# Kernel optimization log

Hardware: AMD Instinct MI355X
Metric: run time of the kernel (lower is better)

Reference implementation:

```python
import jax, jax.numpy as jnp
import numpy as np

B, T, C = 8, 2048, 1024
H, S = 16, 64  # heads, head size (R=K=V=S)
HEAD_SIZE_DIVISOR = 8.0
EPS = 1e-5


def setup_inputs() -> dict:
    key = jax.random.key(0)
    ks = jax.random.split(key, 16)
    n = lambda k, shape, s=1.0: jax.random.normal(k, shape, dtype=jnp.float32) * s
    u = lambda k, shape: jax.random.uniform(k, shape, dtype=jnp.float32)
    w_scale = 0.02
    return {
        "xq": n(ks[0], (B, T, C)),
        "xk": n(ks[1], (B, T, C)),
        "xv": n(ks[2], (B, T, C)),
        "time_mix_k": u(ks[3], (1, 1, C)),
        "time_mix_v": u(ks[4], (1, 1, C)),
        "time_mix_r": u(ks[5], (1, 1, C)),
        "time_mix_g": u(ks[6], (1, 1, C)),
        "time_decay": n(ks[7], (H, S)),          # decay speed logits
        "time_faaaa": u(ks[8], (H, S)) * 0.5,     # per-channel bonus
        "Wr": n(ks[9], (C, C), w_scale),
        "Wk": n(ks[10], (C, C), w_scale),
        "Wv": n(ks[11], (C, C), w_scale),
        "Wg": n(ks[12], (C, C), w_scale),
        "Wo": n(ks[13], (C, C), w_scale),
        "ln_w": jnp.ones((C,), jnp.float32),
        "ln_b": jnp.zeros((C,), jnp.float32),
    }


def reference(xq, xk, xv, time_mix_k, time_mix_v, time_mix_r, time_mix_g,
              time_decay, time_faaaa, Wr, Wk, Wv, Wg, Wo, ln_w, ln_b):
    # Note: the torch forward ignores its xk/xv args and rebuilds them from xq.
    x = xq
    Bx, Tx, Cx = x.shape
    # time_shift: shift sequence right by 1, zero-pad first position
    xs = jnp.concatenate([jnp.zeros_like(x[:, :1]), x[:, :-1]], axis=1)
    mix = lambda m: x * m + xs * (1.0 - m)
    # projections (torch Linear: y = x @ W.T), split into heads
    r = (mix(time_mix_r) @ Wr.T).reshape(Bx, Tx, H, S)
    k = (mix(time_mix_k) @ Wk.T).reshape(Bx, Tx, H, S)
    v = (mix(time_mix_v) @ Wv.T).reshape(Bx, Tx, H, S)
    g = jax.nn.silu(mix(time_mix_g) @ Wg.T)  # (B, T, H*S)

    w = jnp.exp(-jnp.exp(time_decay))[None, :, :, None]  # (1,H,K,1) per-k-channel decay in (0,1)
    u = time_faaaa[None, :, :, None]                      # (1,H,K,1) bonus for current token

    def step(s, rkv):
        rt, kt, vt = rkv  # each (B, H, S)
        at = jnp.einsum('bhk,bhv->bhkv', kt, vt)          # outer product
        out = jnp.einsum('bhk,bhkv->bhv', rt, u * at + s)
        return at + w * s, out

    rkv = (jnp.swapaxes(r, 0, 1).swapaxes(1, 2).transpose(0, 1, 2, 3),) if False else None
    r_t = r.transpose(1, 0, 2, 3)  # (T, B, H, S)
    k_t = k.transpose(1, 0, 2, 3)
    v_t = v.transpose(1, 0, 2, 3)
    s0 = jnp.zeros((Bx, H, S, S), dtype=x.dtype)
    _, out = jax.lax.scan(step, s0, (r_t, k_t, v_t))  # out: (T, B, H, S)
    out = out.transpose(1, 0, 2, 3)  # (B, T, H, S)

    # GroupNorm with num_groups=H over channels H*S, applied to out/8
    y = out / HEAD_SIZE_DIVISOR
    mu = y.mean(axis=-1, keepdims=True)
    var = y.var(axis=-1, keepdims=True)
    y = (y - mu) / jnp.sqrt(var + EPS)
    y = y.reshape(Bx, Tx, H * S) * ln_w + ln_b

    return (y * g) @ Wo.T
```

## Files before the change

kernel.cpp:

```cpp
#include <hip/hip_runtime.h>
#include <stdint.h>

using bf16x8 = __attribute__((ext_vector_type(8))) __bf16;
using f32x4  = __attribute__((ext_vector_type(4))) float;

__device__ __forceinline__ unsigned short f2bf(float f) {
  unsigned u = __float_as_uint(f);
  u = u + 0x7FFFu + ((u >> 16) & 1u);
  return (unsigned short)(u >> 16);
}
__device__ __forceinline__ float bf2f(unsigned short h) {
  return __uint_as_float(((unsigned)h) << 16);
}
__device__ __forceinline__ void gload16(const void* g, void* l) {
  __builtin_amdgcn_global_load_lds((const __attribute__((address_space(1))) void*)g,
                                   (__attribute__((address_space(3))) void*)l, 16, 0, 0);
}

__global__ __launch_bounds__(256) void castw_kernel(const float* __restrict__ w,
                                                    unsigned short* __restrict__ o) {
  int i4 = blockIdx.x * 256 + threadIdx.x;
  float4 f = *(const float4*)(w + (size_t)i4 * 4);
  ushort4 u;
  u.x = f2bf(f.x); u.y = f2bf(f.y); u.z = f2bf(f.z); u.w = f2bf(f.w);
  *(ushort4*)(o + (size_t)i4 * 4) = u;
}

__global__ __launch_bounds__(256) void mix1_kernel(const float* __restrict__ x,
                                                   const float* __restrict__ m,
                                                   unsigned short* __restrict__ amix) {
  int idx = blockIdx.x * 256 + threadIdx.x;
  int row = idx >> 8;
  int c0  = (idx & 255) << 2;
  size_t xoff = (size_t)row * 1024 + c0;
  float4 xv = *(const float4*)(x + xoff);
  float4 xs = make_float4(0.f, 0.f, 0.f, 0.f);
  if ((row & 2047) != 0) xs = *(const float4*)(x + xoff - 1024);
  float4 mm = *(const float4*)(m + c0);
  ushort4 u;
  u.x = f2bf(xv.x * mm.x + xs.x * (1.f - mm.x));
  u.y = f2bf(xv.y * mm.y + xs.y * (1.f - mm.y));
  u.z = f2bf(xv.z * mm.z + xs.z * (1.f - mm.z));
  u.w = f2bf(xv.w * mm.w + xs.w * (1.f - mm.w));
  *(ushort4*)(amix + xoff) = u;
}

__global__ __launch_bounds__(256) void gemm_kernel(
    const unsigned short* __restrict__ A,
    const unsigned short* __restrict__ W,
    unsigned short* __restrict__ Cbf,
    float* __restrict__ Cf,
    int do_silu, int f32out) {
  const int brow = blockIdx.y * 128;
  const int bcol = blockIdx.x * 128;
  const int t = threadIdx.x;
  const int lane = t & 63, wv = t >> 6;
  const int wr = wv >> 1, wc = wv & 1;
  const int lm = lane & 15, lk = lane >> 4;

  __shared__ __align__(16) unsigned short Al[128 * 32];
  __shared__ __align__(16) unsigned short Bl[128 * 32];

  f32x4 acc[4][4];
  const f32x4 z4 = {0.f, 0.f, 0.f, 0.f};
  #pragma unroll
  for (int mi = 0; mi < 4; ++mi)
    #pragma unroll
    for (int ni = 0; ni < 4; ++ni) acc[mi][ni] = z4;

  for (int kt = 0; kt < 32; ++kt) {
    __syncthreads();
    #pragma unroll
    for (int is = 0; is < 2; ++is) {
      int chunk = is * 256 + t;
      int r  = chunk >> 2;
      int c8 = (chunk & 3) << 3;
      int lb = (is * 256 + wv * 64) * 8;
      gload16(A + (size_t)(brow + r) * 1024 + kt * 32 + c8, &Al[lb]);
      gload16(W + (size_t)(bcol + r) * 1024 + kt * 32 + c8, &Bl[lb]);
    }
    __syncthreads();
    bf16x8 af[4], bfv[4];
    #pragma unroll
    for (int mi = 0; mi < 4; ++mi)
      af[mi] = *(const bf16x8*)&Al[(wr * 64 + mi * 16 + lm) * 32 + lk * 8];
    #pragma unroll
    for (int ni = 0; ni < 4; ++ni)
      bfv[ni] = *(const bf16x8*)&Bl[(wc * 64 + ni * 16 + lm) * 32 + lk * 8];
    #pragma unroll
    for (int mi = 0; mi < 4; ++mi)
      #pragma unroll
      for (int ni = 0; ni < 4; ++ni)
        acc[mi][ni] = __builtin_amdgcn_mfma_f32_16x16x32_bf16(af[mi], bfv[ni], acc[mi][ni], 0, 0, 0);
  }

  const int r0 = brow + wr * 64;
  const int c0 = bcol + wc * 64;
  #pragma unroll
  for (int mi = 0; mi < 4; ++mi) {
    #pragma unroll
    for (int ni = 0; ni < 4; ++ni) {
      #pragma unroll
      for (int rg = 0; rg < 4; ++rg) {
        int row = r0 + mi * 16 + lk * 4 + rg;
        int col = c0 + ni * 16 + lm;
        float v = acc[mi][ni][rg];
        if (f32out) {
          Cf[(size_t)row * 1024 + col] = v;
        } else {
          if (do_silu) v = v / (1.f + expf(-v));
          Cbf[(size_t)row * 1024 + col] = f2bf(v);
        }
      }
    }
  }
}

__global__ __launch_bounds__(256) void scan_pass1(
    const unsigned short* __restrict__ kg,
    const unsigned short* __restrict__ vg,
    const float* __restrict__ td,
    float* __restrict__ states) {
  const int c = blockIdx.x, h = blockIdx.y, b = blockIdx.z;
  const int t = threadIdx.x, lane = t & 63, wv = t >> 6;
  float w_i[16], s_i[16];
  #pragma unroll
  for (int i = 0; i < 16; ++i) {
    w_i[i] = expf(-expf(td[h * 64 + wv * 16 + i]));
    s_i[i] = 0.f;
  }
  __shared__ __align__(16) float kb[16][64];
  __shared__ __align__(16) float vb[16][64];
  const int t0 = c * 128;
  for (int q0 = 0; q0 < 128; q0 += 16) {
    __syncthreads();
    {
      int a = t >> 7, rem = t & 127;
      int q = rem >> 3, c8 = (rem & 7) << 3;
      const unsigned short* src = (a == 0) ? kg : vg;
      uint4 u = *(const uint4*)(src + ((size_t)(b * 2048 + t0 + q0 + q) * 16 + h) * 64 + c8);
      float* dst = (a == 0) ? &kb[q][c8] : &vb[q][c8];
      dst[0] = bf2f(u.x & 0xffff); dst[1] = bf2f(u.x >> 16);
      dst[2] = bf2f(u.y & 0xffff); dst[3] = bf2f(u.y >> 16);
      dst[4] = bf2f(u.z & 0xffff); dst[5] = bf2f(u.z >> 16);
      dst[6] = bf2f(u.w & 0xffff); dst[7] = bf2f(u.w >> 16);
    }
    __syncthreads();
    #pragma unroll
    for (int q = 0; q < 16; ++q) {
      float vj = vb[q][lane];
      const float4* kp = (const float4*)&kb[q][wv * 16];
      #pragma unroll
      for (int a4 = 0; a4 < 4; ++a4) {
        float4 k4 = kp[a4];
        s_i[a4*4+0] = fmaf(w_i[a4*4+0], s_i[a4*4+0], k4.x * vj);
        s_i[a4*4+1] = fmaf(w_i[a4*4+1], s_i[a4*4+1], k4.y * vj);
        s_i[a4*4+2] = fmaf(w_i[a4*4+2], s_i[a4*4+2], k4.z * vj);
        s_i[a4*4+3] = fmaf(w_i[a4*4+3], s_i[a4*4+3], k4.w * vj);
      }
    }
  }
  size_t base = (((size_t)(b * 16 + h) * 16 + c) * 64) * 64;
  #pragma unroll
  for (int i = 0; i < 16; ++i)
    states[base + (size_t)(wv * 16 + i) * 64 + lane] = s_i[i];
}

__global__ __launch_bounds__(256) void scan_pass2(const float* __restrict__ td,
                                                  float* __restrict__ states) {
  const int bh = blockIdx.x;
  const int h = bh & 15;
  const int t = threadIdx.x;
  float run[16], wl[16];
  #pragma unroll
  for (int i = 0; i < 16; ++i) {
    int kk = (t + i * 256) >> 6;
    wl[i] = expf(-128.f * expf(td[h * 64 + kk]));
    run[i] = 0.f;
  }
  size_t base0 = (size_t)bh * 16 * 4096;
  for (int c = 0; c < 16; ++c) {
    size_t base = base0 + (size_t)c * 4096;
    #pragma unroll
    for (int i = 0; i < 16; ++i) {
      float tmp = states[base + t + i * 256];
      states[base + t + i * 256] = run[i];
      run[i] = fmaf(wl[i], run[i], tmp);
    }
  }
}

__global__ __launch_bounds__(256) void scan_pass3(
    const unsigned short* __restrict__ rg,
    const unsigned short* __restrict__ kg,
    const unsigned short* __restrict__ vg,
    const float* __restrict__ td,
    const float* __restrict__ fa,
    const float* __restrict__ states,
    float* __restrict__ outb) {
  const int c = blockIdx.x, h = blockIdx.y, b = blockIdx.z;
  const int t = threadIdx.x, lane = t & 63, wv = t >> 6;
  const int kq = lane & 3;
  const int jj = wv * 16 + (lane >> 2);
  float w_i[16], u_i[16], s_i[16];
  size_t sbase = (((size_t)(b * 16 + h) * 16 + c) * 64) * 64;
  #pragma unroll
  for (int i = 0; i < 16; ++i) {
    int kk = kq * 16 + i;
    w_i[i] = expf(-expf(td[h * 64 + kk]));
    u_i[i] = fa[h * 64 + kk];
    s_i[i] = states[sbase + (size_t)kk * 64 + jj];
  }
  __shared__ __align__(16) float rb[16][64];
  __shared__ __align__(16) float kb[16][64];
  __shared__ __align__(16) float vb[16][64];
  const int t0 = c * 128;
  for (int q0 = 0; q0 < 128; q0 += 16) {
    __syncthreads();
    for (int ch = t; ch < 384; ch += 256) {
      int a = ch >> 7, rem = ch & 127;
      int q = rem >> 3, c8 = (rem & 7) << 3;
      const unsigned short* src = (a == 0) ? rg : ((a == 1) ? kg : vg);
      uint4 u = *(const uint4*)(src + ((size_t)(b * 2048 + t0 + q0 + q) * 16 + h) * 64 + c8);
      float* dst = (a == 0) ? &rb[q][c8] : ((a == 1) ? &kb[q][c8] : &vb[q][c8]);
      dst[0] = bf2f(u.x & 0xffff); dst[1] = bf2f(u.x >> 16);
      dst[2] = bf2f(u.y & 0xffff); dst[3] = bf2f(u.y >> 16);
      dst[4] = bf2f(u.z & 0xffff); dst[5] = bf2f(u.z >> 16);
      dst[6] = bf2f(u.w & 0xffff); dst[7] = bf2f(u.w >> 16);
    }
    __syncthreads();
    #pragma unroll
    for (int q = 0; q < 16; ++q) {
      float vj = vb[q][jj];
      const float4* rp = (const float4*)&rb[q][kq * 16];
      const float4* kp = (const float4*)&kb[q][kq * 16];
      float acc = 0.f;
      #pragma unroll
      for (int a4 = 0; a4 < 4; ++a4) {
        float4 r4 = rp[a4], k4 = kp[a4];
        { float kv = k4.x * vj; acc = fmaf(r4.x, fmaf(u_i[a4*4+0], kv, s_i[a4*4+0]), acc); s_i[a4*4+0] = fmaf(w_i[a4*4+0], s_i[a4*4+0], kv); }
        { float kv = k4.y * vj; acc = fmaf(r4.y, fmaf(u_i[a4*4+1], kv, s_i[a4*4+1]), acc); s_i[a4*4+1] = fmaf(w_i[a4*4+1], s_i[a4*4+1], kv); }
        { float kv = k4.z * vj; acc = fmaf(r4.z, fmaf(u_i[a4*4+2], kv, s_i[a4*4+2]), acc); s_i[a4*4+2] = fmaf(w_i[a4*4+2], s_i[a4*4+2], kv); }
        { float kv = k4.w * vj; acc = fmaf(r4.w, fmaf(u_i[a4*4+3], kv, s_i[a4*4+3]), acc); s_i[a4*4+3] = fmaf(w_i[a4*4+3], s_i[a4*4+3], kv); }
      }
      acc += __shfl_xor(acc, 1);
      acc += __shfl_xor(acc, 2);
      if (kq == 0)
        outb[((size_t)(b * 2048 + t0 + q0 + q) * 16 + h) * 64 + jj] = acc;
    }
  }
}

__global__ __launch_bounds__(256) void gnorm_kernel(
    const float* __restrict__ outb,
    const unsigned short* __restrict__ gb,
    const float* __restrict__ lnw,
    const float* __restrict__ lnb,
    unsigned short* __restrict__ a5) {
  const int t = threadIdx.x, lane = t & 63, wv = t >> 6;
  const int grp = blockIdx.x * 4 + wv;
  const int bt = grp >> 4, h = grp & 15;
  const size_t off = (size_t)bt * 1024 + h * 64 + lane;
  float y = outb[off] * 0.125f;
  float s1 = y, s2 = y * y;
  #pragma unroll
  for (int d = 1; d < 64; d <<= 1) {
    s1 += __shfl_xor(s1, d);
    s2 += __shfl_xor(s2, d);
  }
  float mean = s1 * 0.015625f;
  float var  = s2 * 0.015625f - mean * mean;
  float rstd = rsqrtf(var + 1e-5f);
  float yn = (y - mean) * rstd * lnw[h * 64 + lane] + lnb[h * 64 + lane];
  a5[off] = f2bf(yn * bf2f(gb[off]));
}

extern "C" void kernel_launch(void* const* d_in, const int* in_sizes, int n_in,
                              void* d_out, int out_size, void* d_ws, size_t ws_size,
                              hipStream_t stream) {
  const float* xq  = (const float*)d_in[0];
  const float* tmk = (const float*)d_in[3];
  const float* tmv = (const float*)d_in[4];
  const float* tmr = (const float*)d_in[5];
  const float* tmg = (const float*)d_in[6];
  const float* td  = (const float*)d_in[7];
  const float* fa  = (const float*)d_in[8];
  const float* lnw = (const float*)d_in[14];
  const float* lnb = (const float*)d_in[15];

  char* ws = (char*)d_ws;
  unsigned short* WBF  = (unsigned short*)(ws);
  char*           SCR  = ws + 10485760ull;
  unsigned short* RKVG = (unsigned short*)(ws + 44040192ull);
  unsigned short* AMIX = (unsigned short*)SCR;
  float*          ST   = (float*)SCR;
  unsigned short* A5   = (unsigned short*)SCR;
  float*          OUTB = (float*)d_out;

  for (int i = 0; i < 5; ++i)
    castw_kernel<<<1024, 256, 0, stream>>>((const float*)d_in[9 + i], WBF + (size_t)i * 1048576);

  const float* mixes[4] = {tmr, tmk, tmv, tmg};
  for (int z = 0; z < 4; ++z) {
    mix1_kernel<<<16384, 256, 0, stream>>>(xq, mixes[z], AMIX);
    gemm_kernel<<<dim3(8, 128), 256, 0, stream>>>(AMIX, WBF + (size_t)z * 1048576,
                                                  RKVG + (size_t)z * 16777216, (float*)nullptr,
                                                  (z == 3) ? 1 : 0, 0);
  }

  scan_pass1<<<dim3(16, 16, 8), 256, 0, stream>>>(RKVG + 16777216ull, RKVG + 33554432ull, td, ST);
  scan_pass2<<<128, 256, 0, stream>>>(td, ST);
  scan_pass3<<<dim3(16, 16, 8), 256, 0, stream>>>(RKVG, RKVG + 16777216ull, RKVG + 33554432ull,
                                                  td, fa, ST, OUTB);

  gnorm_kernel<<<65536, 256, 0, stream>>>(OUTB, RKVG + 50331648ull, lnw, lnb, A5);

  gemm_kernel<<<dim3(8, 128), 256, 0, stream>>>(A5, WBF + 4194304ull,
                                                (unsigned short*)nullptr, (float*)d_out, 0, 1);
}
```

Before: 833.2 us.

## Use MFMA for chunk state, fuse group norm into scan, merge weight casts

The chunk-state pass now computes each chunk's end state as one bf16 matrix product on MFMA. The keys are pre-scaled by decay powers and both operands are stored transposed in swizzled shared memory, replacing the per-step FMA recurrence. The group norm and gating step is fused into the output scan pass, which writes the gated bf16 result in place over the g buffer. This removes the separate gnorm kernel and the fp32 round trip through global memory. The five weight-cast launches are merged into one, and the chunk states now carry bf16 rounding error on decay-scaled keys.

```diff
diff --git a/kernel.cpp b/kernel.cpp
--- a/kernel.cpp
+++ b/kernel.cpp
@@ -17,13 +17,17 @@
                                    (__attribute__((address_space(3))) void*)l, 16, 0, 0);
 }
 
-__global__ __launch_bounds__(256) void castw_kernel(const float* __restrict__ w,
-                                                    unsigned short* __restrict__ o) {
+__global__ __launch_bounds__(256) void castw5_kernel(
+    const float* __restrict__ w0, const float* __restrict__ w1,
+    const float* __restrict__ w2, const float* __restrict__ w3,
+    const float* __restrict__ w4, unsigned short* __restrict__ o) {
+  const float* wsrc[5] = {w0, w1, w2, w3, w4};
+  const float* w = wsrc[blockIdx.y];
   int i4 = blockIdx.x * 256 + threadIdx.x;
   float4 f = *(const float4*)(w + (size_t)i4 * 4);
   ushort4 u;
   u.x = f2bf(f.x); u.y = f2bf(f.y); u.z = f2bf(f.z); u.w = f2bf(f.w);
-  *(ushort4*)(o + (size_t)i4 * 4) = u;
+  *(ushort4*)(o + (size_t)blockIdx.y * 1048576 + (size_t)i4 * 4) = u;
 }
 
 __global__ __launch_bounds__(256) void mix1_kernel(const float* __restrict__ x,
@@ -123,47 +127,66 @@
     float* __restrict__ states) {
   const int c = blockIdx.x, h = blockIdx.y, b = blockIdx.z;
   const int t = threadIdx.x, lane = t & 63, wv = t >> 6;
-  float w_i[16], s_i[16];
-  #pragma unroll
-  for (int i = 0; i < 16; ++i) {
-    w_i[i] = expf(-expf(td[h * 64 + wv * 16 + i]));
-    s_i[i] = 0.f;
-  }
-  __shared__ __align__(16) float kb[16][64];
-  __shared__ __align__(16) float vb[16][64];
+  __shared__ __align__(16) unsigned short kwT[64 * 128];
+  __shared__ __align__(16) unsigned short vT[64 * 128];
+
+  const int a  = t & 7;
+  const int d0 = a * 8;
+  const int sb = t >> 3;
+  float eta[8];
+  #pragma unroll
+  for (int j = 0; j < 8; ++j) eta[j] = expf(td[h * 64 + d0 + j]);
   const int t0 = c * 128;
-  for (int q0 = 0; q0 < 128; q0 += 16) {
-    __syncthreads();
-    {
-      int a = t >> 7, rem = t & 127;
-      int q = rem >> 3, c8 = (rem & 7) << 3;
-      const unsigned short* src = (a == 0) ? kg : vg;
-      uint4 u = *(const uint4*)(src + ((size_t)(b * 2048 + t0 + q0 + q) * 16 + h) * 64 + c8);
-      float* dst = (a == 0) ? &kb[q][c8] : &vb[q][c8];
-      dst[0] = bf2f(u.x & 0xffff); dst[1] = bf2f(u.x >> 16);
-      dst[2] = bf2f(u.y & 0xffff); dst[3] = bf2f(u.y >> 16);
-      dst[4] = bf2f(u.z & 0xffff); dst[5] = bf2f(u.z >> 16);
-      dst[6] = bf2f(u.w & 0xffff); dst[7] = bf2f(u.w >> 16);
-    }
-    __syncthreads();
-    #pragma unroll
-    for (int q = 0; q < 16; ++q) {
-      float vj = vb[q][lane];
-      const float4* kp = (const float4*)&kb[q][wv * 16];
-      #pragma unroll
-      for (int a4 = 0; a4 < 4; ++a4) {
-        float4 k4 = kp[a4];
-        s_i[a4*4+0] = fmaf(w_i[a4*4+0], s_i[a4*4+0], k4.x * vj);
-        s_i[a4*4+1] = fmaf(w_i[a4*4+1], s_i[a4*4+1], k4.y * vj);
-        s_i[a4*4+2] = fmaf(w_i[a4*4+2], s_i[a4*4+2], k4.z * vj);
-        s_i[a4*4+3] = fmaf(w_i[a4*4+3], s_i[a4*4+3], k4.w * vj);
-      }
+  #pragma unroll
+  for (int i = 0; i < 4; ++i) {
+    int s = sb + 32 * i;
+    size_t goff = ((size_t)(b * 2048 + t0 + s) * 16 + h) * 64 + d0;
+    uint4 ku = *(const uint4*)(kg + goff);
+    uint4 vu = *(const uint4*)(vg + goff);
+    unsigned short kv[8] = {(unsigned short)(ku.x & 0xffff), (unsigned short)(ku.x >> 16),
+                            (unsigned short)(ku.y & 0xffff), (unsigned short)(ku.y >> 16),
+                            (unsigned short)(ku.z & 0xffff), (unsigned short)(ku.z >> 16),
+                            (unsigned short)(ku.w & 0xffff), (unsigned short)(ku.w >> 16)};
+    unsigned short vv[8] = {(unsigned short)(vu.x & 0xffff), (unsigned short)(vu.x >> 16),
+                            (unsigned short)(vu.y & 0xffff), (unsigned short)(vu.y >> 16),
+                            (unsigned short)(vu.z & 0xffff), (unsigned short)(vu.z >> 16),
+                            (unsigned short)(vu.w & 0xffff), (unsigned short)(vu.w >> 16)};
+    float p = -(float)(127 - s);
+    int ss = s ^ (a << 3);
+    #pragma unroll
+    for (int j = 0; j < 8; ++j) {
+      float wpow = expf(p * eta[j]);
+      kwT[(d0 + j) * 128 + ss] = f2bf(bf2f(kv[j]) * wpow);
+      vT [(d0 + j) * 128 + ss] = vv[j];
+    }
+  }
+  __syncthreads();
+
+  const int lm = lane & 15, lk = lane >> 4;
+  const int aR = (wv * 2 + (lm >> 3)) & 7;
+  f32x4 acc[4];
+  const f32x4 z4 = {0.f, 0.f, 0.f, 0.f};
+  #pragma unroll
+  for (int ni = 0; ni < 4; ++ni) acc[ni] = z4;
+  #pragma unroll
+  for (int ks = 0; ks < 4; ++ks) {
+    bf16x8 af = *(const bf16x8*)&kwT[(wv * 16 + lm) * 128 + (((ks * 4 + lk) ^ aR) << 3)];
+    #pragma unroll
+    for (int ni = 0; ni < 4; ++ni) {
+      int aV = (ni * 2 + (lm >> 3)) & 7;
+      bf16x8 bv = *(const bf16x8*)&vT[(ni * 16 + lm) * 128 + (((ks * 4 + lk) ^ aV) << 3)];
+      acc[ni] = __builtin_amdgcn_mfma_f32_16x16x32_bf16(af, bv, acc[ni], 0, 0, 0);
     }
   }
   size_t base = (((size_t)(b * 16 + h) * 16 + c) * 64) * 64;
   #pragma unroll
-  for (int i = 0; i < 16; ++i)
-    states[base + (size_t)(wv * 16 + i) * 64 + lane] = s_i[i];
+  for (int ni = 0; ni < 4; ++ni)
+    #pragma unroll
+    for (int rg = 0; rg < 4; ++rg) {
+      int row = wv * 16 + lk * 4 + rg;
+      int col = ni * 16 + lm;
+      states[base + (size_t)row * 64 + col] = acc[ni][rg];
+    }
 }
 
 __global__ __launch_bounds__(256) void scan_pass2(const float* __restrict__ td,
@@ -197,7 +220,9 @@
     const float* __restrict__ td,
     const float* __restrict__ fa,
     const float* __restrict__ states,
-    float* __restrict__ outb) {
+    const float* __restrict__ lnw,
+    const float* __restrict__ lnb,
+    unsigned short* gbuf ) {
   const int c = blockIdx.x, h = blockIdx.y, b = blockIdx.z;
   const int t = threadIdx.x, lane = t & 63, wv = t >> 6;
   const int kq = lane & 3;
@@ -214,6 +239,7 @@
   __shared__ __align__(16) float rb[16][64];
   __shared__ __align__(16) float kb[16][64];
   __shared__ __align__(16) float vb[16][64];
+  __shared__ __align__(16) float ob[16][64];
   const int t0 = c * 128;
   for (int q0 = 0; q0 < 128; q0 += 16) {
     __syncthreads();
@@ -245,34 +271,38 @@
       }
       acc += __shfl_xor(acc, 1);
       acc += __shfl_xor(acc, 2);
-      if (kq == 0)
-        outb[((size_t)(b * 2048 + t0 + q0 + q) * 16 + h) * 64 + jj] = acc;
-    }
-  }
-}
-
-__global__ __launch_bounds__(256) void gnorm_kernel(
-    const float* __restrict__ outb,
-    const unsigned short* __restrict__ gb,
-    const float* __restrict__ lnw,
-    const float* __restrict__ lnb,
-    unsigned short* __restrict__ a5) {
-  const int t = threadIdx.x, lane = t & 63, wv = t >> 6;
-  const int grp = blockIdx.x * 4 + wv;
-  const int bt = grp >> 4, h = grp & 15;
-  const size_t off = (size_t)bt * 1024 + h * 64 + lane;
-  float y = outb[off] * 0.125f;
-  float s1 = y, s2 = y * y;
-  #pragma unroll
-  for (int d = 1; d < 64; d <<= 1) {
-    s1 += __shfl_xor(s1, d);
-    s2 += __shfl_xor(s2, d);
-  }
-  float mean = s1 * 0.015625f;
-  float var  = s2 * 0.015625f - mean * mean;
-  float rstd = rsqrtf(var + 1e-5f);
-  float yn = (y - mean) * rstd * lnw[h * 64 + lane] + lnb[h * 64 + lane];
-  a5[off] = f2bf(yn * bf2f(gb[off]));
+      if (kq == 0) ob[q][jj] = acc;
+    }
+    __syncthreads();
+    {
+      int r  = wv * 4 + (lane >> 4);
+      int c4 = (lane & 15) * 4;
+      float4 y4 = *(const float4*)&ob[r][c4];
+      y4.x *= 0.125f; y4.y *= 0.125f; y4.z *= 0.125f; y4.w *= 0.125f;
+      float s1 = y4.x + y4.y + y4.z + y4.w;
+      float s2 = y4.x * y4.x + y4.y * y4.y + y4.z * y4.z + y4.w * y4.w;
+      #pragma unroll
+      for (int d = 1; d < 16; d <<= 1) {
+        s1 += __shfl_xor(s1, d);
+        s2 += __shfl_xor(s2, d);
+      }
+      float mean = s1 * 0.015625f;
+      float var  = s2 * 0.015625f - mean * mean;
+      float rstd = rsqrtf(var + 1e-5f);
+      float4 lw = *(const float4*)(lnw + h * 64 + c4);
+      float4 lb = *(const float4*)(lnb + h * 64 + c4);
+      size_t go = ((size_t)(b * 2048 + t0 + q0 + r) * 16 + h) * 64 + c4;
+      uint2 gu = *(const uint2*)(gbuf + go);
+      float g0 = bf2f(gu.x & 0xffff), g1 = bf2f(gu.x >> 16);
+      float g2 = bf2f(gu.y & 0xffff), g3 = bf2f(gu.y >> 16);
+      ushort4 o;
+      o.x = f2bf(((y4.x - mean) * rstd * lw.x + lb.x) * g0);
+      o.y = f2bf(((y4.y - mean) * rstd * lw.y + lb.y) * g1);
+      o.z = f2bf(((y4.z - mean) * rstd * lw.z + lb.z) * g2);
+      o.w = f2bf(((y4.w - mean) * rstd * lw.w + lb.w) * g3);
+      *(ushort4*)(gbuf + go) = o;
+    }
+  }
 }
 
 extern "C" void kernel_launch(void* const* d_in, const int* in_sizes, int n_in,
@@ -294,11 +324,10 @@
   unsigned short* RKVG = (unsigned short*)(ws + 44040192ull);
   unsigned short* AMIX = (unsigned short*)SCR;
   float*          ST   = (float*)SCR;
-  unsigned short* A5   = (unsigned short*)SCR;
-  float*          OUTB = (float*)d_out;
-
-  for (int i = 0; i < 5; ++i)
-    castw_kernel<<<1024, 256, 0, stream>>>((const float*)d_in[9 + i], WBF + (size_t)i * 1048576);
+
+  castw5_kernel<<<dim3(1024, 5), 256, 0, stream>>>(
+      (const float*)d_in[9], (const float*)d_in[10], (const float*)d_in[11],
+      (const float*)d_in[12], (const float*)d_in[13], WBF);
 
   const float* mixes[4] = {tmr, tmk, tmv, tmg};
   for (int z = 0; z < 4; ++z) {
@@ -311,10 +340,8 @@
   scan_pass1<<<dim3(16, 16, 8), 256, 0, stream>>>(RKVG + 16777216ull, RKVG + 33554432ull, td, ST);
   scan_pass2<<<128, 256, 0, stream>>>(td, ST);
   scan_pass3<<<dim3(16, 16, 8), 256, 0, stream>>>(RKVG, RKVG + 16777216ull, RKVG + 33554432ull,
-                                                  td, fa, ST, OUTB);
-
-  gnorm_kernel<<<65536, 256, 0, stream>>>(OUTB, RKVG + 50331648ull, lnw, lnb, A5);
-
-  gemm_kernel<<<dim3(8, 128), 256, 0, stream>>>(A5, WBF + 4194304ull,
+                                                  td, fa, ST, lnw, lnb, RKVG + 50331648ull);
+
+  gemm_kernel<<<dim3(8, 128), 256, 0, stream>>>(RKVG + 50331648ull, WBF + 4194304ull,
                                                 (unsigned short*)nullptr, (float*)d_out, 0, 1);
 }
```

Measured after the change: 748.1 us. 1.11x faster.
